# Performance work log

Hardware: AMD Instinct MI355X
Metric: run time of the kernel (lower is better)

## Reference

```python
import jax, jax.numpy as jnp
import numpy as np

H_DIM = 1024
N_HEADS = 16
HEAD_D = H_DIM // N_HEADS  # 64


def setup_inputs() -> dict:
    key = jax.random.key(0)
    ks = jax.random.split(key, 10)
    B, T, C = 2, 2048, H_DIM
    init = 1.0 / np.sqrt(C)  # lecun_normal-scale stand-in
    src = jax.random.normal(ks[0], (B, T, C), dtype=jnp.float32)
    mask = jnp.ones((B, T), dtype=jnp.float32)  # unused when causal
    Wq = jax.random.normal(ks[1], (C, H_DIM), dtype=jnp.float32) * init
    Wk = jax.random.normal(ks[2], (C, H_DIM), dtype=jnp.float32) * init
    Wv = jax.random.normal(ks[3], (C, H_DIM), dtype=jnp.float32) * init
    Wo = jax.random.normal(ks[4], (H_DIM, H_DIM), dtype=jnp.float32) * init
    bq = jnp.zeros((H_DIM,), jnp.float32)
    bk = jnp.zeros((H_DIM,), jnp.float32)
    bv = jnp.zeros((H_DIM,), jnp.float32)
    bo = jnp.zeros((H_DIM,), jnp.float32)
    return {"src": src, "mask": mask, "Wq": Wq, "bq": bq, "Wk": Wk, "bk": bk,
            "Wv": Wv, "bv": bv, "Wo": Wo, "bo": bo}


def reference(src, mask, Wq, bq, Wk, bk, Wv, bv, Wo, bo):
    # MaskedCausalAttention forward, deterministic=True (dropout = identity),
    # use_causal_mask=True.
    B, T, C = src.shape
    N, D = N_HEADS, HEAD_D
    # q,k,v: [B, N, T, D]
    q = (src @ Wq + bq).reshape(B, T, N, D).transpose(0, 2, 1, 3)
    k = (src @ Wk + bk).reshape(B, T, N, D).transpose(0, 2, 1, 3)
    v = (src @ Wv + bv).reshape(B, T, N, D).transpose(0, 2, 1, 3)
    # scores: [B, N, T, T]
    scores = jnp.einsum('bntd,bnsd->bnts', q, k) / jnp.sqrt(jnp.float32(D))
    causal = jnp.tril(jnp.ones((T, T), dtype=bool))[None, None]
    scores = jnp.where(causal, scores, -jnp.inf)
    probs = jax.nn.softmax(scores, axis=-1)
    attn = jnp.einsum('bnts,bnsd->bntd', probs, v)  # [B, N, T, D]
    attn = attn.transpose(0, 2, 1, 3).reshape(B, T, N * D)
    return attn @ Wo + bo
```

## Files before the change

kernel.cpp:

```cpp
#include <hip/hip_runtime.h>
#include <hip/hip_bf16.h>

typedef __hip_bfloat16 bf16;
typedef __attribute__((ext_vector_type(8))) short short8;
typedef __attribute__((ext_vector_type(4))) float f32x4;

#define BATCH 2
#define SEQ   2048
#define HDIM  1024
#define NHEAD 16
#define DHEAD 64
#define MROWS (BATCH*SEQ)

#define QSCALE 0.18033688f
#define EXP2F(x) __builtin_amdgcn_exp2f(x)

static __device__ __forceinline__ short f2bs(float x) {
    __hip_bfloat16 h = (__hip_bfloat16)x;
    return *reinterpret_cast<short*>(&h);
}
static __device__ __forceinline__ unsigned int pk2(float a, float b) {
    __hip_bfloat162 h = __float22bfloat162_rn(make_float2(a, b));
    return *reinterpret_cast<unsigned int*>(&h);
}

static __device__ __forceinline__ void gload16(const void* g, void* l) {
    __builtin_amdgcn_global_load_lds(
        (const __attribute__((address_space(1))) unsigned int*)g,
        (__attribute__((address_space(3))) unsigned int*)l, 16, 0, 0);
}

__global__ __launch_bounds__(256) void prep1(const float* __restrict__ src,
        const float* __restrict__ Wq, const float* __restrict__ Wk,
        const float* __restrict__ Wv, const float* __restrict__ Wo,
        short* __restrict__ Sb, short* __restrict__ WT,
        short* __restrict__ WoT)
{
    __shared__ float t[64][65];
    const int bx = blockIdx.x, tid = threadIdx.x;
    if (bx < 4096) {
        int i = bx * 256 + tid;
        float4 v = ((const float4*)src)[i];
        ushort4 o;
        o.x = (unsigned short)f2bs(v.x);
        o.y = (unsigned short)f2bs(v.y);
        o.z = (unsigned short)f2bs(v.z);
        o.w = (unsigned short)f2bs(v.w);
        ((ushort4*)Sb)[i] = o;
        return;
    }
    const int tb = bx - 4096;
    const int wsel = tb >> 8;
    const float* W = (wsel == 0) ? Wq : (wsel == 1) ? Wk : (wsel == 2) ? Wv : Wo;
    short* dst = (wsel < 3) ? WT : WoT;
    const int roff = (wsel < 3) ? wsel * 1024 : 0;
    const int t8 = tb & 255;
    const int n0 = (t8 & 15) * 64, k0 = (t8 >> 4) * 64;
#pragma unroll
    for (int i = 0; i < 16; i++) {
        int idx = tid + i * 256, r = idx >> 6, c = idx & 63;
        t[r][c] = W[(size_t)(k0 + r) * HDIM + n0 + c];
    }
    __syncthreads();
#pragma unroll
    for (int i = 0; i < 16; i++) {
        int idx = tid + i * 256, c = idx >> 6, r = idx & 63;
        dst[(size_t)(roff + n0 + c) * HDIM + k0 + r] = f2bs(t[r][c]);
    }
}

__global__ __launch_bounds__(512, 2) void gemm_qkv(const short* __restrict__ A,
        const short* __restrict__ Bt,
        const float* __restrict__ bq, const float* __restrict__ bk,
        const float* __restrict__ bv,
        short* __restrict__ Qout, short* __restrict__ Kout,
        short* __restrict__ Vtout)
{
    __shared__ short SM[2][32768];
    const int tid = threadIdx.x, lane = tid & 63, w = tid >> 6;
    const int quad = lane >> 4, l15 = lane & 15;
    const int m0 = blockIdx.y * 256, n0 = blockIdx.x * 256;
    const int wr = w >> 1, wc = w & 1;

    const short* gp[4][2];
    int lo[4][2];
#pragma unroll
    for (int g = 0; g < 4; g++)
#pragma unroll
        for (int i = 0; i < 2; i++) {
            if (g < 2) {
                int u = g * 16 + w * 2 + i;
                gp[g][i] = A + (size_t)(m0 + (u >> 1) * 16 + l15) * HDIM
                             + (u & 1) * 32 + quad * 8;
                lo[g][i] = u * 512;
            } else {
                int j = w * 2 + i;
                int v = (g == 2 ? 0 : 8) + j + (j >= 8 ? 8 : 0);
                gp[g][i] = Bt + (size_t)(n0 + (v >> 1) * 16 + l15) * HDIM
                              + (v & 1) * 32 + quad * 8;
                lo[g][i] = 16384 + v * 512;
            }
        }

    f32x4 acc[4][8];
#pragma unroll
    for (int i = 0; i < 4; i++)
#pragma unroll
        for (int j = 0; j < 8; j++) acc[i][j] = (f32x4){0.f, 0.f, 0.f, 0.f};

#pragma unroll
    for (int g = 0; g < 4; g++)
#pragma unroll
        for (int i = 0; i < 2; i++) { gload16(gp[g][i], &SM[0][lo[g][i]]); gp[g][i] += 64; }

    short8 af[4][2];
    for (int t = 0; t < 16; ++t) {
        const short* Tb = SM[t & 1];
        short* Sn = SM[(t + 1) & 1];

        asm volatile("s_waitcnt vmcnt(2)" ::: "memory");
        __builtin_amdgcn_s_barrier();
#pragma unroll
        for (int mi = 0; mi < 4; mi++)
#pragma unroll
            for (int kh = 0; kh < 2; kh++)
                af[mi][kh] = *(const short8*)
                    &Tb[((wr * 4 + mi) * 2 + kh) * 512 + lane * 8];
        short8 bf01[4][2];
#pragma unroll
        for (int nn = 0; nn < 4; nn++)
#pragma unroll
            for (int kh = 0; kh < 2; kh++)
                bf01[nn][kh] = *(const short8*)
                    &Tb[16384 + ((wc * 8 + nn) * 2 + kh) * 512 + lane * 8];

        if (t < 15) {
#pragma unroll
            for (int g = 0; g < 4; g++)
#pragma unroll
                for (int i = 0; i < 2; i++) { gload16(gp[g][i], Sn + lo[g][i]); gp[g][i] += 64; }
        }

        __builtin_amdgcn_s_setprio(1);
#pragma unroll
        for (int nn = 0; nn < 4; nn++)
#pragma unroll
            for (int mi = 0; mi < 4; mi++)
#pragma unroll
                for (int kh = 0; kh < 2; kh++)
                    acc[mi][nn] = __builtin_amdgcn_mfma_f32_16x16x32_bf16(
                        af[mi][kh], bf01[nn][kh], acc[mi][nn], 0, 0, 0);
        __builtin_amdgcn_s_setprio(0);

        if (t < 15) asm volatile("s_waitcnt vmcnt(8)" ::: "memory");
        else        asm volatile("s_waitcnt vmcnt(0)" ::: "memory");

        short8 bf23[4][2];
#pragma unroll
        for (int nn = 0; nn < 4; nn++)
#pragma unroll
            for (int kh = 0; kh < 2; kh++)
                bf23[nn][kh] = *(const short8*)
                    &Tb[16384 + ((wc * 8 + 4 + nn) * 2 + kh) * 512 + lane * 8];

        __builtin_amdgcn_s_setprio(1);
#pragma unroll
        for (int nn = 0; nn < 4; nn++)
#pragma unroll
            for (int mi = 0; mi < 4; mi++)
#pragma unroll
                for (int kh = 0; kh < 2; kh++)
                    acc[mi][4 + nn] = __builtin_amdgcn_mfma_f32_16x16x32_bf16(
                        af[mi][kh], bf23[nn][kh], acc[mi][4 + nn], 0, 0, 0);
        __builtin_amdgcn_s_setprio(0);
    }

    const int region = blockIdx.x >> 2;
    if (region < 2) {
        const float* bias = region ? bk : bq;
        const float oscale = region ? 1.0f : QSCALE;
        short* C = region ? Kout : Qout;
#pragma unroll
        for (int mi = 0; mi < 4; mi++) {
            int mB = m0 + wr * 64 + mi * 16 + quad * 4;
#pragma unroll
            for (int ni = 0; ni < 8; ni++) {
                int nl = (n0 + (wc * 8 + ni) * 16 + l15) & 1023;
                float bb = bias[nl];
#pragma unroll
                for (int r = 0; r < 4; r++)
                    C[(size_t)(mB + r) * HDIM + nl] =
                        f2bs((acc[mi][ni][r] + bb) * oscale);
            }
        }
    } else {
#pragma unroll
        for (int mi = 0; mi < 4; mi++) {
            int mB = m0 + wr * 64 + mi * 16 + quad * 4;
            int bb = mB >> 11, tt = mB & 2047;
#pragma unroll
            for (int ni = 0; ni < 8; ni++) {
                int n = n0 + (wc * 8 + ni) * 16 + l15;
                int h = (n >> 6) & 15, d = n & 63;
                float bvv = bv[n & 1023];
                size_t base = ((size_t)((bb * NHEAD + h) * DHEAD + d)) * SEQ + tt;
                ushort4 pk;
                pk.x = (unsigned short)f2bs(acc[mi][ni][0] + bvv);
                pk.y = (unsigned short)f2bs(acc[mi][ni][1] + bvv);
                pk.z = (unsigned short)f2bs(acc[mi][ni][2] + bvv);
                pk.w = (unsigned short)f2bs(acc[mi][ni][3] + bvv);
                *(ushort4*)(Vtout + base) = pk;
            }
        }
    }
}

__global__ __launch_bounds__(512) void attn_mfma(const short* __restrict__ Qb,
        const short* __restrict__ Kb, const short* __restrict__ Vt,
        short* __restrict__ Ab)
{
    __shared__ short SMEM[25600];
    const int tid = threadIdx.x, lane = tid & 63, w = tid >> 6;
    const int quad = lane >> 4, l15 = lane & 15;
    const int L = blockIdx.x;

    const int pair = (L & 7) + 8 * ((L >> 3) & 3);
    const int sblk = 15 - (L >> 5);
    const int b = pair >> 4, head = pair & 15;
    const int nj = 2 * sblk + 2;

    const short* Kbh = Kb + (size_t)b * SEQ * HDIM + head * DHEAD;
    const short* Vth = Vt + (size_t)(b * NHEAD + head) * DHEAD * SEQ;
    short* Pw = SMEM + 16384 + w * 1152;

    const int s_w = 2 * sblk + (w >> 2);
    const int qr = sblk * 128 + w * 16 + l15;

    const short* qptr = Qb + (size_t)(b * SEQ + qr) * HDIM + head * DHEAD + quad * 8;
    short8 bq0 = *(const short8*)qptr;
    short8 bq1 = *(const short8*)(qptr + 32);

    const short* gp[2];
    int stp[2], ldo[2];
#pragma unroll
    for (int i = 0; i < 2; i++) {
        int c8 = w * 2 + i;
        if (c8 < 8) {
            int t = c8 >> 1, h = c8 & 1;
            gp[i] = Kbh + (size_t)(t * 16 + l15) * HDIM + h * 32 + quad * 8;
            stp[i] = 64 * HDIM;
        } else {
            int c = c8 - 8, dt = c >> 1, kh = c & 1;
            gp[i] = Vth + (size_t)(dt * 16 + l15) * SEQ + kh * 32 + quad * 8;
            stp[i] = 64;
        }
        ldo[i] = c8 * 512;
    }

    f32x4 o[4];
#pragma unroll
    for (int dt = 0; dt < 4; dt++) o[dt] = (f32x4){0.f, 0.f, 0.f, 0.f};
    float psum = 0.f;

#pragma unroll
    for (int i = 0; i < 2; i++) { gload16(gp[i], &SMEM[ldo[i]]); gp[i] += stp[i]; }

    for (int j = 0; j < nj; ++j) {
        const int cur = j & 1;
        short* Ks = &SMEM[cur * 8192];
        short* Vs = Ks + 4096;

        if (j + 1 < nj) {
            short* nb = &SMEM[(cur ^ 1) * 8192];
#pragma unroll
            for (int i = 0; i < 2; i++) { gload16(gp[i], nb + ldo[i]); gp[i] += stp[i]; }
            asm volatile("s_waitcnt vmcnt(2)" ::: "memory");
        } else {
            asm volatile("s_waitcnt vmcnt(0)" ::: "memory");
        }
        __builtin_amdgcn_s_barrier();

        const int s0 = j * 64;
        f32x4 sv[4];
        __builtin_amdgcn_s_setprio(1);
#pragma unroll
        for (int t = 0; t < 4; t++) {
            sv[t] = (f32x4){0.f, 0.f, 0.f, 0.f};
            short8 k0 = *(const short8*)&Ks[(t * 2) * 512 + lane * 8];
            short8 k1 = *(const short8*)&Ks[(t * 2 + 1) * 512 + lane * 8];
            sv[t] = __builtin_amdgcn_mfma_f32_16x16x32_bf16(k0, bq0, sv[t], 0, 0, 0);
            sv[t] = __builtin_amdgcn_mfma_f32_16x16x32_bf16(k1, bq1, sv[t], 0, 0, 0);
        }
        __builtin_amdgcn_s_setprio(0);

        float p[16];
        if (j >= s_w) {
#pragma unroll
            for (int t = 0; t < 4; t++)
#pragma unroll
                for (int r = 0; r < 4; r++) {
                    int key = s0 + t * 16 + quad * 4 + r;
                    p[t * 4 + r] = (key <= qr) ? EXP2F(sv[t][r]) : 0.f;
                }
        } else {
#pragma unroll
            for (int t = 0; t < 4; t++)
#pragma unroll
                for (int r = 0; r < 4; r++)
                    p[t * 4 + r] = EXP2F(sv[t][r]);
        }
#pragma unroll
        for (int i = 0; i < 16; i++) psum += p[i];

#pragma unroll
        for (int t = 0; t < 4; t++) {
            uint2 u2;
            u2.x = pk2(p[t * 4],     p[t * 4 + 1]);
            u2.y = pk2(p[t * 4 + 2], p[t * 4 + 3]);
            *(uint2*)&Pw[l15 * 72 + t * 16 + quad * 4] = u2;
        }
        short8 bp0 = *(const short8*)&Pw[l15 * 72 + quad * 8];
        short8 bp1 = *(const short8*)&Pw[l15 * 72 + 32 + quad * 8];

        __builtin_amdgcn_s_setprio(1);
#pragma unroll
        for (int dt = 0; dt < 4; dt++) {
            short8 av0 = *(const short8*)&Vs[(dt * 2) * 512 + lane * 8];
            short8 av1 = *(const short8*)&Vs[(dt * 2 + 1) * 512 + lane * 8];
            o[dt] = __builtin_amdgcn_mfma_f32_16x16x32_bf16(av0, bp0, o[dt], 0, 0, 0);
            o[dt] = __builtin_amdgcn_mfma_f32_16x16x32_bf16(av1, bp1, o[dt], 0, 0, 0);
        }
        __builtin_amdgcn_s_setprio(0);
        __builtin_amdgcn_s_barrier();
    }

    float lrow = psum + __shfl_xor(psum, 16);
    lrow += __shfl_xor(lrow, 32);
    const float inv = 1.f / lrow;

    const size_t obase = (size_t)(b * SEQ + qr) * HDIM + head * DHEAD;
#pragma unroll
    for (int dt = 0; dt < 4; dt++) {
        uint2 u2;
        u2.x = pk2(o[dt][0] * inv, o[dt][1] * inv);
        u2.y = pk2(o[dt][2] * inv, o[dt][3] * inv);
        *(uint2*)&Ab[obase + dt * 16 + quad * 4] = u2;
    }
}

__global__ __launch_bounds__(512) void gemm_o(const short* __restrict__ A,
        const short* __restrict__ Bt, const float* __restrict__ bo,
        float* __restrict__ Out)
{
    __shared__ short SM[2 * 16384];
    const int tid = threadIdx.x, lane = tid & 63, w = tid >> 6;
    const int quad = lane >> 4, l15 = lane & 15;
    const int m0 = blockIdx.y * 128, n0 = blockIdx.x * 128;
    const int wr = w >> 2, wc = w & 3;

    const short* gsrc[4];
    short* ldst[4];
#pragma unroll
    for (int i = 0; i < 4; i++) {
        int c8 = w * 4 + i;
        if (c8 < 16) {
            gsrc[i] = A + (size_t)(m0 + (c8 >> 1) * 16 + l15) * HDIM
                        + (c8 & 1) * 32 + quad * 8;
            ldst[i] = &SM[c8 * 512];
        } else {
            int v = c8 - 16;
            gsrc[i] = Bt + (size_t)(n0 + (v >> 1) * 16 + l15) * HDIM
                         + (v & 1) * 32 + quad * 8;
            ldst[i] = &SM[8192 + v * 512];
        }
    }

    f32x4 acc[4][2];
#pragma unroll
    for (int i = 0; i < 4; i++)
#pragma unroll
        for (int j = 0; j < 2; j++) acc[i][j] = (f32x4){0.f, 0.f, 0.f, 0.f};

#pragma unroll
    for (int i = 0; i < 4; i++) { gload16(gsrc[i], ldst[i]); gsrc[i] += 64; }

    for (int kk = 0; kk < 16; ++kk) {
        const int cur = kk & 1;
        if (kk < 15) {
            const int nb = (cur ^ 1) * 16384;
#pragma unroll
            for (int i = 0; i < 4; i++) { gload16(gsrc[i], ldst[i] + nb); gsrc[i] += 64; }
            asm volatile("s_waitcnt vmcnt(4)" ::: "memory");
        } else {
            asm volatile("s_waitcnt vmcnt(0)" ::: "memory");
        }
        __builtin_amdgcn_s_barrier();

        const short* Asb = &SM[cur * 16384];
        const short* Bsb = Asb + 8192;
#pragma unroll
        for (int kh = 0; kh < 2; kh++) {
            short8 af[4], bfr[2];
#pragma unroll
            for (int mi = 0; mi < 4; mi++)
                af[mi] = *(const short8*)&Asb[((wr * 4 + mi) * 2 + kh) * 512 + lane * 8];
#pragma unroll
            for (int ni = 0; ni < 2; ni++)
                bfr[ni] = *(const short8*)&Bsb[((wc * 2 + ni) * 2 + kh) * 512 + lane * 8];
#pragma unroll
            for (int mi = 0; mi < 4; mi++)
#pragma unroll
                for (int ni = 0; ni < 2; ni++)
                    acc[mi][ni] = __builtin_amdgcn_mfma_f32_16x16x32_bf16(
                                      af[mi], bfr[ni], acc[mi][ni], 0, 0, 0);
        }
        __builtin_amdgcn_s_barrier();
    }

#pragma unroll
    for (int mi = 0; mi < 4; mi++) {
        int mB = m0 + (wr * 4 + mi) * 16 + quad * 4;
#pragma unroll
        for (int ni = 0; ni < 2; ni++) {
            int n = n0 + (wc * 2 + ni) * 16 + l15;
            float bb = bo[n];
#pragma unroll
            for (int r = 0; r < 4; r++)
                Out[(size_t)(mB + r) * HDIM + n] = acc[mi][ni][r] + bb;
        }
    }
}

extern "C" void kernel_launch(void* const* d_in, const int* in_sizes, int n_in,
                              void* d_out, int out_size, void* d_ws, size_t ws_size,
                              hipStream_t stream)
{
    const float* src = (const float*)d_in[0];
    const float* Wq = (const float*)d_in[2];
    const float* bq = (const float*)d_in[3];
    const float* Wk = (const float*)d_in[4];
    const float* bk = (const float*)d_in[5];
    const float* Wv = (const float*)d_in[6];
    const float* bv = (const float*)d_in[7];
    const float* Wo = (const float*)d_in[8];
    const float* bo = (const float*)d_in[9];
    float* out = (float*)d_out;

    short* Sb   = (short*)d_ws;
    short* Qb   = Sb + (size_t)MROWS * HDIM;
    short* Kb   = Qb + (size_t)MROWS * HDIM;
    short* Vt   = Kb + (size_t)MROWS * HDIM;
    short* WoT  = Vt + (size_t)MROWS * HDIM;
    short* WT   = (short*)d_out;
    short* Ab   = Qb;

    prep1<<<dim3(4096 + 1024), dim3(256), 0, stream>>>(src, Wq, Wk, Wv, Wo, Sb, WT, WoT);

    gemm_qkv<<<dim3(12, 16), dim3(512), 0, stream>>>(Sb, WT, bq, bk, bv, Qb, Kb, Vt);

    attn_mfma<<<dim3(512), dim3(512), 0, stream>>>(Qb, Kb, Vt, Ab);

    gemm_o<<<dim3(8, 32), dim3(512), 0, stream>>>(Ab, WoT, bo, out);
}
```

Measured before the change: 195.2 us.

## Split long causal attention query blocks across two workgroups with combine pass

The causal attention kernel now splits the key range for the longer query blocks (sblk 8-15) into two halves processed by separate workgroups, raising the grid from 512 to 768 blocks to balance the triangular workload. Partial unnormalized outputs and row sums are written to fp32 scratch (reusing output and staging buffers), and a new combine kernel adds the halves, normalizes, and writes bf16. This targets tail imbalance and low occupancy from long causal rows, at the cost of extra global traffic and an additional kernel launch.

```diff
diff --git a/kernel.cpp b/kernel.cpp
--- a/kernel.cpp
+++ b/kernel.cpp
@@ -217,24 +217,35 @@
 
 __global__ __launch_bounds__(512) void attn_mfma(const short* __restrict__ Qb,
         const short* __restrict__ Kb, const short* __restrict__ Vt,
-        short* __restrict__ Ab)
+        short* __restrict__ Ab,
+        float* __restrict__ Opart, float* __restrict__ Psum)
 {
     __shared__ short SMEM[25600];
     const int tid = threadIdx.x, lane = tid & 63, w = tid >> 6;
     const int quad = lane >> 4, l15 = lane & 15;
     const int L = blockIdx.x;
 
+    static const signed char S_TAB[24] =
+        {15,15, 7,14,14,13,13, 6,12,12,11,11, 5,10,10, 9, 9, 4, 8, 8, 3, 2, 1, 0};
+    static const signed char H_TAB[24] =
+        { 0, 1,-1, 0, 1, 0, 1,-1, 0, 1, 0, 1,-1, 0, 1, 0, 1,-1, 0, 1,-1,-1,-1,-1};
+
     const int pair = (L & 7) + 8 * ((L >> 3) & 3);
-    const int sblk = 15 - (L >> 5);
+    const int u = L >> 5;
     const int b = pair >> 4, head = pair & 15;
-    const int nj = 2 * sblk + 2;
+    const int sblk = S_TAB[u];
+    const int half = H_TAB[u];
+    const int it0   = (half == 1) ? (sblk + 1) : 0;
+    const int itEnd = (half == 0) ? (sblk + 1) : (2 * sblk + 2);
+    const int nj = itEnd - it0;
 
     const short* Kbh = Kb + (size_t)b * SEQ * HDIM + head * DHEAD;
     const short* Vth = Vt + (size_t)(b * NHEAD + head) * DHEAD * SEQ;
     short* Pw = SMEM + 16384 + w * 1152;
 
     const int s_w = 2 * sblk + (w >> 2);
-    const int qr = sblk * 128 + w * 16 + l15;
+    const int rho = w * 16 + l15;
+    const int qr = sblk * 128 + rho;
 
     const short* qptr = Qb + (size_t)(b * SEQ + qr) * HDIM + head * DHEAD + quad * 8;
     short8 bq0 = *(const short8*)qptr;
@@ -255,6 +266,7 @@
             stp[i] = 64;
         }
         ldo[i] = c8 * 512;
+        gp[i] += (size_t)it0 * stp[i];
     }
 
     f32x4 o[4];
@@ -280,7 +292,8 @@
         }
         __builtin_amdgcn_s_barrier();
 
-        const int s0 = j * 64;
+        const int itg = it0 + j;
+        const int s0 = itg * 64;
         f32x4 sv[4];
         __builtin_amdgcn_s_setprio(1);
 #pragma unroll
@@ -294,7 +307,7 @@
         __builtin_amdgcn_s_setprio(0);
 
         float p[16];
-        if (j >= s_w) {
+        if (itg >= s_w) {
 #pragma unroll
             for (int t = 0; t < 4; t++)
 #pragma unroll
@@ -336,8 +349,18 @@
 
     float lrow = psum + __shfl_xor(psum, 16);
     lrow += __shfl_xor(lrow, 32);
+
+    if (half >= 0) {
+        const int tile = (pair * 8 + (sblk - 8)) * 2 + half;
+        float* Ot = Opart + (size_t)tile * 8192;
+#pragma unroll
+        for (int dt = 0; dt < 4; dt++)
+            *(f32x4*)&Ot[rho * 64 + dt * 16 + quad * 4] = o[dt];
+        if (quad == 0) Psum[(pair * 8 + (sblk - 8)) * 256 + half * 128 + rho] = lrow;
+        return;
+    }
+
     const float inv = 1.f / lrow;
-
     const size_t obase = (size_t)(b * SEQ + qr) * HDIM + head * DHEAD;
 #pragma unroll
     for (int dt = 0; dt < 4; dt++) {
@@ -345,6 +368,36 @@
         u2.x = pk2(o[dt][0] * inv, o[dt][1] * inv);
         u2.y = pk2(o[dt][2] * inv, o[dt][3] * inv);
         *(uint2*)&Ab[obase + dt * 16 + quad * 4] = u2;
+    }
+}
+
+__global__ __launch_bounds__(256) void combine(const float* __restrict__ Opart,
+        const float* __restrict__ Psum, short* __restrict__ Ab)
+{
+    const int bxx = blockIdx.x;
+    const int pair = bxx & 31, si = bxx >> 5;
+    const int b = pair >> 4, head = pair & 15;
+    const int tid = threadIdx.x;
+    const int row = tid >> 1, dq = (tid & 1) * 32;
+
+    const size_t t0 = ((size_t)(pair * 8 + si) * 2) * 8192;
+    const float* O0 = Opart + t0;
+    const float* O1 = O0 + 8192;
+    const int p0 = (pair * 8 + si) * 256;
+    const float inv = 1.f / (Psum[p0 + row] + Psum[p0 + 128 + row]);
+
+    const int qrow = (8 + si) * 128 + row;
+    const size_t obase = (size_t)(b * SEQ + qrow) * HDIM + head * DHEAD + dq;
+#pragma unroll
+    for (int g = 0; g < 8; g++) {
+        float4 a = *(const float4*)&O0[row * 64 + dq + g * 4];
+        float4 c = *(const float4*)&O1[row * 64 + dq + g * 4];
+        ushort4 pk;
+        pk.x = (unsigned short)f2bs((a.x + c.x) * inv);
+        pk.y = (unsigned short)f2bs((a.y + c.y) * inv);
+        pk.z = (unsigned short)f2bs((a.z + c.z) * inv);
+        pk.w = (unsigned short)f2bs((a.w + c.w) * inv);
+        *(ushort4*)&Ab[obase + g * 4] = pk;
     }
 }
 
@@ -453,12 +506,16 @@
     short* WoT  = Vt + (size_t)MROWS * HDIM;
     short* WT   = (short*)d_out;
     short* Ab   = Qb;
+    float* Opart = (float*)d_out;
+    float* Psum  = (float*)Sb;
 
     prep1<<<dim3(4096 + 1024), dim3(256), 0, stream>>>(src, Wq, Wk, Wv, Wo, Sb, WT, WoT);
 
     gemm_qkv<<<dim3(12, 16), dim3(512), 0, stream>>>(Sb, WT, bq, bk, bv, Qb, Kb, Vt);
 
-    attn_mfma<<<dim3(512), dim3(512), 0, stream>>>(Qb, Kb, Vt, Ab);
+    attn_mfma<<<dim3(768), dim3(512), 0, stream>>>(Qb, Kb, Vt, Ab, Opart, Psum);
+
+    combine<<<dim3(256), dim3(256), 0, stream>>>(Opart, Psum, Ab);
 
     gemm_o<<<dim3(8, 32), dim3(512), 0, stream>>>(Ab, WoT, bo, out);
 }
```

New measurement: 193.6 us. No clear change (-0.8%).
